# Kernel optimization log

Measured on AMD Instinct MI355X. Metric: run time of the kernel, lower is better.

## Reference

```python
import jax, jax.numpy as jnp
import numpy as np

B, L, D = 2, 2048, 1024
D_INNER, DT_RANK, D_STATE, D_CONV = 2048, 64, 16, 4


def setup_inputs() -> dict:
    key = jax.random.key(0)
    ks = jax.random.split(key, 10)
    x = jax.random.normal(ks[0], (B, L, D), jnp.float32)
    W_in = jax.random.normal(ks[1], (2 * D_INNER, D), jnp.float32) * (1.0 / np.sqrt(D))
    conv_w = jax.random.normal(ks[2], (D_INNER, 1, D_CONV), jnp.float32) * 0.5
    conv_b = jax.random.normal(ks[3], (D_INNER,), jnp.float32) * 0.1
    W_x = jax.random.normal(ks[4], (DT_RANK + 2 * D_STATE, D_INNER), jnp.float32) * (1.0 / np.sqrt(D_INNER))
    W_dt = jax.random.normal(ks[5], (D_INNER, DT_RANK), jnp.float32) * (1.0 / np.sqrt(DT_RANK))
    b_dt = jax.random.normal(ks[6], (D_INNER,), jnp.float32) * 0.1
    W_out = jax.random.normal(ks[7], (D, D_INNER), jnp.float32) * (1.0 / np.sqrt(D_INNER))
    # S4D-real style init: A_log = log(1..N) per channel
    A_log = jnp.log(jnp.tile(jnp.arange(1, D_STATE + 1, dtype=jnp.float32), (D_INNER, 1)))
    D_skip = jnp.ones((D_INNER,), jnp.float32)
    return {"x": x, "W_in": W_in, "conv_w": conv_w, "conv_b": conv_b,
            "W_x": W_x, "W_dt": W_dt, "b_dt": b_dt, "W_out": W_out,
            "A_log": A_log, "D_skip": D_skip}


def _selective_scan(xi, dt, A, Bm, Cm, D_skip):
    # xi, dt: (B,L,Di); A: (Di,N); Bm,Cm: (B,L,N); D_skip: (Di,)
    dA = jnp.exp(dt[..., None] * A)                       # (B,L,Di,N)
    dBx = dt[..., None] * Bm[:, :, None, :] * xi[..., None]  # (B,L,Di,N)

    def combine(e1, e2):
        a1, b1 = e1
        a2, b2 = e2
        return a1 * a2, a2 * b1 + b2

    _, h = jax.lax.associative_scan(combine, (dA, dBx), axis=1)  # (B,L,Di,N)
    y = jnp.einsum('bldn,bln->bld', h, Cm)
    return y + D_skip * xi


def reference(x, W_in, conv_w, conv_b, W_x, W_dt, b_dt, W_out, A_log, D_skip):
    Lq = x.shape[1]
    xz = x @ W_in.T                                   # (B,L,2*Di)
    xi, z = jnp.split(xz, 2, axis=-1)
    # causal depthwise conv over time
    xc = jnp.transpose(xi, (0, 2, 1))                 # (B,Di,L)
    xc = jax.lax.conv_general_dilated(
        xc, conv_w, window_strides=(1,), padding=[(D_CONV - 1, 0)],
        dimension_numbers=('NCH', 'OIH', 'NCH'), feature_group_count=D_INNER)
    xc = xc + conv_b[None, :, None]
    xi = jnp.transpose(xc, (0, 2, 1))[:, :Lq]         # (B,L,Di)
    xi = jax.nn.silu(xi)
    x_dbl = xi @ W_x.T                                # (B,L,dt_rank+2N)
    dt, B_ssm, C_ssm = jnp.split(x_dbl, [DT_RANK, DT_RANK + D_STATE], axis=-1)
    dt = jax.nn.softplus(dt @ W_dt.T + b_dt)          # (B,L,Di)
    A = -jnp.exp(A_log.astype(jnp.float32))
    y = _selective_scan(xi, dt, A, B_ssm, C_ssm, D_skip.astype(jnp.float32))
    return (y * jax.nn.silu(z)) @ W_out.T
```

## Files before the change

kernel.cpp:

```cpp
#include <hip/hip_runtime.h>
#include <math.h>

typedef float          floatx4  __attribute__((ext_vector_type(4)));
typedef unsigned int   uintx4   __attribute__((ext_vector_type(4)));
typedef unsigned short ushortx4 __attribute__((ext_vector_type(4)));
typedef unsigned short u16;

constexpr int Bq  = 2;
constexpr int Lq  = 2048;
constexpr int Dq  = 1024;
constexpr int DI  = 2048;
constexpr int DTR = 64;
constexpr int NST = 16;
constexpr int MR  = Bq * Lq;

constexpr size_t NWB     = (size_t)MR * DI;
constexpr size_t W_XIPRE = 0;
constexpr size_t W_Z     = NWB;
constexpr size_t W_XDBL  = 2 * NWB;
constexpr size_t SZ_XDBL = (size_t)MR * 96;
constexpr size_t SZ_PS16 = (size_t)Bq * 16 * NST * DI;
constexpr size_t W_PB    = W_XDBL + SZ_XDBL;
constexpr size_t W_SB    = W_PB + SZ_PS16;
constexpr size_t W_R1    = W_SB + SZ_PS16;
constexpr size_t W_SM    = W_R1 + NWB;
constexpr size_t U_WDT = 524288, U_WX = 655360;
constexpr size_t SM_F32  = 425984;
constexpr size_t W_PS2   = W_SM + SM_F32;
__host__ __device__ constexpr size_t SZPS(int nc) { return (size_t)Bq * nc * NST * DI; }
__host__ __device__ constexpr size_t SZR(int nc)  { return (size_t)Bq * nc * DI; }

__device__ __forceinline__ u16 f2b(float x) {
    unsigned int u = __float_as_uint(x);
    u += 0x7fffu + ((u >> 16) & 1u);
    return (u16)(u >> 16);
}
__device__ __forceinline__ float b2f(u16 h) { return __uint_as_float(((unsigned int)h) << 16); }
__device__ __forceinline__ float silu_f(float x) { return x / (1.f + __expf(-x)); }

__device__ __forceinline__ void mfma16(floatx4& d, uintx4 a, uintx4 b) {
    asm("v_mfma_f32_16x16x32_bf16 %0, %1, %2, %0" : "+v"(d) : "v"(a), "v"(b));
}
__device__ __forceinline__ void gload16(const void* g, void* l) {
    __builtin_amdgcn_global_load_lds((const __attribute__((address_space(1))) void*)g,
                                     (__attribute__((address_space(3))) void*)l, 16, 0, 0);
}

__device__ __forceinline__ void pow_ladder(float r, float dA[NST]) {
    float r2 = r * r;
    float e4 = r2 * r2;
    dA[0] = r; dA[1] = r2; dA[2] = r2 * r; dA[3] = e4;
#pragma unroll
    for (int n = 4; n < NST; n++) dA[n] = dA[n - 4] * e4;
}
__device__ __forceinline__ void dA_ladder(float dtv, float dA[NST]) {
    pow_ladder(__expf(-dtv), dA);
}
__device__ __forceinline__ float pow_m(float R, int m) {
    float r2 = R * R, r4 = r2 * r2, r8 = r4 * r4, r16 = r8 * r8;
    float p = 1.f;
    if (m & 1)  p *= R;
    if (m & 2)  p *= r2;
    if (m & 4)  p *= r4;
    if (m & 8)  p *= r8;
    if (m & 16) p *= r16;
    return p;
}

__device__ __forceinline__ void split_store(const floatx4 v, u16* hi, u16* lo, size_t t) {
    ushortx4 h, l;
#pragma unroll
    for (int i = 0; i < 4; i++) {
        h[i] = f2b(v[i]);
        l[i] = f2b(v[i] - b2f(h[i]));
    }
    ((ushortx4*)hi)[t] = h;
    ((ushortx4*)lo)[t] = l;
}
__device__ __forceinline__ void round_store(const floatx4 v, u16* hi, size_t t) {
    ushortx4 h;
#pragma unroll
    for (int i = 0; i < 4; i++) h[i] = f2b(v[i]);
    ((ushortx4*)hi)[t] = h;
}

__global__ __launch_bounds__(256)
void prep(const float* __restrict__ x, u16* __restrict__ xhi,
          const float* __restrict__ W_in, u16* __restrict__ winh,
          const float* __restrict__ W_x, u16* __restrict__ wxh,
          const float* __restrict__ W_dt, u16* __restrict__ wdth,
          float* __restrict__ xdbl,
          const float* __restrict__ W_out, u16* __restrict__ wouth)
{
    int t = blockIdx.x * 256 + threadIdx.x;
    if (t < 1048576) { round_store(((const floatx4*)x)[t], xhi, t); return; }
    t -= 1048576;
    if (t < 1048576) { round_store(((const floatx4*)W_in)[t], winh, t); return; }
    t -= 1048576;
    if (t < 49152)   { round_store(((const floatx4*)W_x)[t], wxh, t); return; }
    t -= 49152;
    if (t < 32768)   { round_store(((const floatx4*)W_dt)[t], wdth, t); return; }
    t -= 32768;
    if (t < 98304)   { ((floatx4*)xdbl)[t] = (floatx4){0.f, 0.f, 0.f, 0.f}; return; }
    t -= 98304;
    if (wouth && t < 524288) round_store(((const floatx4*)W_out)[t], wouth, t);
}

__global__ __launch_bounds__(256)
void round_bf16(const float* __restrict__ src, u16* __restrict__ hi, int n4)
{
    int t = blockIdx.x * 256 + threadIdx.x;
    if (t < n4) round_store(((const floatx4*)src)[t], hi, t);
}

__device__ __forceinline__ void stage64(const u16* g, u16* s, int rows, int ld,
                                        int k0, int wave, int lane)
{
    const int chunks = rows * 8;
    for (int c0 = wave * 64; c0 < chunks; c0 += 256) {
        int c   = c0 + lane;
        int row = c >> 3;
        int kcg = (c & 7) ^ (row & 7);
        const u16* gp = g + (size_t)row * ld + k0 + kcg * 8;
        gload16(gp, s + (size_t)c0 * 8);
    }
}

__device__ __forceinline__ void stageA_f32(const float* g, u16* sh, u16* sl,
                                           int rows, int ldf, int k0, int tid)
{
    const int chunks = rows * 8;
    for (int c = tid; c < chunks; c += 256) {
        int row = c >> 3, kc = c & 7;
        const float* gp = g + (size_t)row * ldf + k0 + kc * 8;
        floatx4 v0 = *(const floatx4*)gp;
        floatx4 v1 = *(const floatx4*)(gp + 4);
        float v[8] = {v0[0], v0[1], v0[2], v0[3], v1[0], v1[1], v1[2], v1[3]};
        unsigned int hh[8], ll[8];
#pragma unroll
        for (int i = 0; i < 8; i++) {
            u16 h = f2b(v[i]);
            hh[i] = h;
            ll[i] = f2b(v[i] - b2f(h));
        }
        uintx4 ph, pl;
#pragma unroll
        for (int i = 0; i < 4; i++) {
            ph[i] = hh[2 * i] | (hh[2 * i + 1] << 16);
            pl[i] = ll[2 * i] | (ll[2 * i + 1] << 16);
        }
        int sc = kc ^ (row & 7);
        *(uintx4*)(sh + (size_t)row * 64 + sc * 8) = ph;
        *(uintx4*)(sl + (size_t)row * 64 + sc * 8) = pl;
    }
}

template <int WM, int WN, int FM, int FN, int EPI, int AF32, int TERMS>
__global__ __launch_bounds__(256)
void gemm2t(const u16* __restrict__ Ah, const u16* __restrict__ Al,
            const u16* __restrict__ Bh,
            float* __restrict__ C, u16* __restrict__ C2u,
            const float* __restrict__ bias,
            const float* __restrict__ Af,
            int M, int N, int K, int lda, int ldb, int ldc, int nsplit)
{
    constexpr int BM = WM * FM * 16, BN = WN * FN * 16, BK = 64;
    __shared__ u16 sm[(TERMS * BM + BN) * BK];
    u16* sAh = sm;
    u16* sAl = sm + BM * BK;
    u16* sBh = sm + TERMS * BM * BK;

    const int tid = threadIdx.x, lane = tid & 63, wave = tid >> 6;
    const int wm = wave % WM, wn = wave / WM;
    const long m0 = (long)blockIdx.y * BM, n0 = (long)blockIdx.x * BN;
    const int frr = lane & 15;

    const int kchunk = K / gridDim.z;
    const int kBeg = blockIdx.z * kchunk;
    const int kEnd = kBeg + kchunk;

    floatx4 acc[FM][FN];
#pragma unroll
    for (int i = 0; i < FM; i++)
#pragma unroll
        for (int j = 0; j < FN; j++) acc[i][j] = (floatx4){0.f, 0.f, 0.f, 0.f};

    const u16* gAh = Ah + (AF32 ? 0 : (size_t)m0 * lda);
    const u16* gAl = Al + (AF32 ? 0 : (size_t)m0 * lda);
    const float* gAf = AF32 ? (Af + (size_t)m0 * lda) : nullptr;
    const u16* gBh = Bh + (size_t)n0 * ldb;

    for (int k0 = kBeg; k0 < kEnd; k0 += BK) {
        if constexpr (AF32) {
            stageA_f32(gAf, sAh, sAl, BM, lda, k0, tid);
        } else {
            stage64(gAh, sAh, BM, lda, k0, wave, lane);
            if constexpr (TERMS == 2)
                stage64(gAl, sAl, BM, lda, k0, wave, lane);
        }
        stage64(gBh, sBh, BN, ldb, k0, wave, lane);
        __syncthreads();

#pragma unroll
        for (int kk = 0; kk < 2; kk++) {
            const int kc = kk * 4 + (lane >> 4);
            uintx4 af[FM], bb[FN];
#pragma unroll
            for (int f = 0; f < FN; f++) {
                int r = (wn * FN + f) * 16 + frr;
                bb[f] = *(const uintx4*)(sBh + r * 64 + (kc ^ (r & 7)) * 8);
            }
#pragma unroll
            for (int f = 0; f < FM; f++) {
                int r = (wm * FM + f) * 16 + frr;
                af[f] = *(const uintx4*)(sAh + r * 64 + (kc ^ (r & 7)) * 8);
            }
#pragma unroll
            for (int fm = 0; fm < FM; fm++)
#pragma unroll
                for (int fn = 0; fn < FN; fn++)
                    mfma16(acc[fm][fn], af[fm], bb[fn]);
            if constexpr (TERMS == 2) {
#pragma unroll
                for (int f = 0; f < FM; f++) {
                    int r = (wm * FM + f) * 16 + frr;
                    af[f] = *(const uintx4*)(sAl + r * 64 + (kc ^ (r & 7)) * 8);
                }
#pragma unroll
                for (int fm = 0; fm < FM; fm++)
#pragma unroll
                    for (int fn = 0; fn < FN; fn++)
                        mfma16(acc[fm][fn], af[fm], bb[fn]);
            }
        }
        __syncthreads();
    }

#pragma unroll
    for (int fm = 0; fm < FM; fm++) {
        long row0 = m0 + (wm * FM + fm) * 16 + ((lane >> 4) << 2);
#pragma unroll
        for (int fn = 0; fn < FN; fn++) {
            long col = n0 + (wn * FN + fn) * 16 + (lane & 15);
#pragma unroll
            for (int i = 0; i < 4; i++) {
                long row = row0 + i;
                float v = acc[fm][fn][i];
                if constexpr (EPI == 1) {
                    v += bias[col];
                    v = (v > 20.f) ? v : log1pf(__expf(v));
                    C[row * (long)ldc + col] = v;
                } else if constexpr (EPI == 2) {
                    if (col < nsplit) C[row * (long)nsplit + col] = v;
                    else              C2u[row * (long)nsplit + (col - nsplit)] = f2b(v);
                } else if constexpr (EPI == 3) {
                    atomicAdd(&C[row * (long)ldc + col], v);
                } else {
                    C[row * (long)ldc + col] = v;
                }
            }
        }
    }
}

__global__ __launch_bounds__(256)
void conv_silu_split(const float* __restrict__ xi_pre, const float* __restrict__ cw,
                     const float* __restrict__ cb, u16* __restrict__ xih,
                     u16* __restrict__ xil)
{
    int t = blockIdx.x * 256 + threadIdx.x;
    int d4 = (t & 511) * 4;
    int l  = (t >> 9) & (Lq - 1);
    int b  = t >> 20;
    const float* base = xi_pre + ((size_t)b * Lq) * DI + d4;
    floatx4 w0 = *(const floatx4*)(cw + (size_t)(d4 + 0) * 4);
    floatx4 w1 = *(const floatx4*)(cw + (size_t)(d4 + 1) * 4);
    floatx4 w2 = *(const floatx4*)(cw + (size_t)(d4 + 2) * 4);
    floatx4 w3 = *(const floatx4*)(cw + (size_t)(d4 + 3) * 4);
    floatx4 o  = *(const floatx4*)(cb + d4);
#pragma unroll
    for (int j = 0; j < 4; j++) {
        int ls = l - 3 + j;
        if (ls < 0) continue;
        floatx4 xv = *(const floatx4*)(base + (size_t)ls * DI);
        o[0] = fmaf(w0[j], xv[0], o[0]);
        o[1] = fmaf(w1[j], xv[1], o[1]);
        o[2] = fmaf(w2[j], xv[2], o[2]);
        o[3] = fmaf(w3[j], xv[3], o[3]);
    }
    size_t oidx = ((size_t)b * Lq + l) * DI + d4;
    ushortx4 h, lo;
#pragma unroll
    for (int i = 0; i < 4; i++) {
        float v = silu_f(o[i]);
        h[i]  = f2b(v);
        lo[i] = f2b(v - b2f(h[i]));
    }
    *(ushortx4*)(xih + oidx) = h;
    *(ushortx4*)(xil + oidx) = lo;
}

template <int NCT>
__global__ __launch_bounds__(256)
void scanAY(const u16* __restrict__ xih, u16* xil ,
            const float* __restrict__ dt,
            const float* __restrict__ xdbl, const float* __restrict__ Dsk,
            u16* __restrict__ Rl16, float* __restrict__ Rend,
            float* __restrict__ S)
{
    constexpr int CLT = Lq / NCT;
    constexpr int CSH = (NCT == 64) ? 6 : (NCT == 32) ? 5 : 4;
    const int tid = threadIdx.x;
    int t = blockIdx.x * 256 + tid;
    int d = t & (DI - 1);
    int c = (t >> 11) & (NCT - 1);
    int b = t >> (11 + CSH);

    __shared__ float sBC[CLT][32];
    int l0 = c * CLT;
    {
        size_t rb = ((size_t)b * Lq + l0) * 96 + DTR;
        for (int i = tid; i < CLT * 32; i += 256) {
            int l = i >> 5, e = i & 31;
            sBC[l][e] = xdbl[rb + (size_t)l * 96 + e];
        }
    }
    __syncthreads();

    float Dv = Dsk[d];
    float h[NST];
#pragma unroll
    for (int n = 0; n < NST; n++) h[n] = 0.f;
    float R = 1.f;

    size_t xbase = ((size_t)b * Lq + l0) * DI + d;
    for (int l = 0; l < CLT; l++) {
        size_t idx = xbase + (size_t)l * DI;
        float dtv = dt[idx];
        float xiv = b2f(xih[idx]) + b2f(xil[idx]);
        float dx  = dtv * xiv;
        float dA[NST];
        dA_ladder(dtv, dA);
        R *= dA[0];
        float y = 0.f;
#pragma unroll
        for (int n = 0; n < NST; n++) {
            h[n] = fmaf(dA[n], h[n], dx * sBC[l][n]);
            y = fmaf(h[n], sBC[l][16 + n], y);
        }
        y = fmaf(Dv, xiv, y);
        xil[idx]  = f2b(y);
        Rl16[idx] = f2b(R);
    }
    Rend[((size_t)(b * NCT + c)) * DI + d] = R;
    size_t obase = ((size_t)(b * NCT + c) * NST) * DI + d;
#pragma unroll
    for (int n = 0; n < NST; n++)
        S[obase + (size_t)n * DI] = h[n];
}

template <int NCT>
__global__ __launch_bounds__(256)
void scanBt(const float* __restrict__ Rend, const float* S, float* Hin)
{
    int t = blockIdx.x * 256 + threadIdx.x;
    int d = t & (DI - 1);
    int n = (t >> 11) & (NST - 1);
    int b = t >> 15;
    const int m = n + 1;
    float H = 0.f;
    for (int c = 0; c < NCT; c++) {
        float R = Rend[((size_t)(b * NCT + c)) * DI + d];
        float p = pow_m(R, m);
        size_t idx = (((size_t)(b * NCT + c) * NST) + n) * DI + d;
        float s = S[idx];
        Hin[idx] = H;
        H = fmaf(p, H, s);
    }
}

template <int NCT>
__global__ __launch_bounds__(256)
void scanCY(u16* __restrict__ xgh,
            const u16* __restrict__ yloc16, const u16* __restrict__ Rl16,
            const float* __restrict__ xdbl,
            const float* __restrict__ Hin, const u16* __restrict__ z)
{
    constexpr int CLT = Lq / NCT;
    constexpr int CSH = (NCT == 64) ? 6 : (NCT == 32) ? 5 : 4;
    const int tid = threadIdx.x;
    int t = blockIdx.x * 256 + tid;
    int d = t & (DI - 1);
    int c = (t >> 11) & (NCT - 1);
    int b = t >> (11 + CSH);

    __shared__ float sC[CLT][NST];
    int l0 = c * CLT;
    {
        size_t rb = ((size_t)b * Lq + l0) * 96 + DTR + NST;
        for (int i = tid; i < CLT * NST; i += 256) {
            int l = i >> 4, e = i & 15;
            sC[l][e] = xdbl[rb + (size_t)l * 96 + e];
        }
    }
    __syncthreads();

    float w[NST];
    size_t hbase = ((size_t)(b * NCT + c) * NST) * DI + d;
#pragma unroll
    for (int n = 0; n < NST; n++) w[n] = Hin[hbase + (size_t)n * DI];

    size_t xbase = ((size_t)b * Lq + l0) * DI + d;
    for (int l = 0; l < CLT; l++) {
        size_t idx = xbase + (size_t)l * DI;
        float yv = b2f(yloc16[idx]);
        float Rv = b2f(Rl16[idx]);
        float pw[NST];
        pow_ladder(Rv, pw);
        float corr = 0.f;
#pragma unroll
        for (int n = 0; n < NST; n++)
            corr = fmaf(w[n] * pw[n], sC[l][n], corr);
        float y = yv + corr;
        float g = y * silu_f(b2f(z[idx]));
        xgh[idx] = f2b(g);
    }
}

extern "C" void kernel_launch(void* const* d_in, const int* in_sizes, int n_in,
                              void* d_out, int out_size, void* d_ws, size_t ws_size,
                              hipStream_t stream)
{
    const float* x      = (const float*)d_in[0];
    const float* W_in   = (const float*)d_in[1];
    const float* conv_w = (const float*)d_in[2];
    const float* conv_b = (const float*)d_in[3];
    const float* W_x    = (const float*)d_in[4];
    const float* W_dt   = (const float*)d_in[5];
    const float* b_dt   = (const float*)d_in[6];
    const float* W_out  = (const float*)d_in[7];
    const float* D_skip = (const float*)d_in[9];
    float* out = (float*)d_out;

    float* ws     = (float*)d_ws;
    float* xi_pre = ws + W_XIPRE;
    float* dt     = xi_pre;
    u16*   zb     = (u16*)(ws + W_Z);
    u16*   Rl16   = zb + NWB;
    float* xdbl   = ws + W_XDBL;
    u16* r1   = (u16*)(ws + W_R1);
    u16* xhi  = r1, *winh = r1 + 4194304;
    u16* xih  = r1, *xil = r1 + 8388608;
    u16* smal = (u16*)(ws + W_SM);
    u16* wdth = smal + U_WDT, *wxh = smal + U_WX;
    u16* wouth = (u16*)(ws + W_PB);

    int nc = 16;
    float *Rend, *Sb;
    if (ws_size >= (W_PS2 + SZR(64) + SZPS(64)) * 4) {
        nc = 64;  Rend = ws + W_PS2; Sb = Rend + SZR(64);
    } else if (ws_size >= (W_PS2 + SZR(32) + SZPS(32)) * 4) {
        nc = 32;  Rend = ws + W_PS2; Sb = Rend + SZR(32);
    } else {
        Rend = ws + W_PB; Sb = ws + W_SB;
    }
    const bool early_wout = (nc >= 32);

    prep<<<early_wout ? 10944 : 8896, 256, 0, stream>>>(
        x, xhi, W_in, winh, W_x, wxh, W_dt, wdth, xdbl,
        W_out, early_wout ? wouth : nullptr);
    gemm2t<2, 2, 4, 4, 2, 0, 1><<<dim3(32, 32), 256, 0, stream>>>(
        xhi, nullptr, winh, xi_pre, zb, nullptr, nullptr, MR, 4096, Dq, Dq, Dq, 2048, 2048);
    conv_silu_split<<<8192, 256, 0, stream>>>(xi_pre, conv_w, conv_b, xih, xil);
    gemm2t<2, 2, 4, 3, 3, 0, 2><<<dim3(1, 32, 8), 256, 0, stream>>>(
        xih, xil, wxh, xdbl, nullptr, nullptr, nullptr, MR, 96, DI, DI, DI, 96, 0);
    gemm2t<2, 2, 4, 4, 1, 1, 2><<<dim3(16, 32), 256, 0, stream>>>(
        nullptr, nullptr, wdth, dt, nullptr, b_dt, xdbl, MR, DI, DTR, 96, DTR, DI, 0);
    if (nc == 64) {
        scanAY<64><<<dim3(Bq * 64 * DI / 256), 256, 0, stream>>>(
            xih, xil, dt, xdbl, D_skip, Rl16, Rend, Sb);
        scanBt<64><<<dim3(Bq * NST * DI / 256), 256, 0, stream>>>(Rend, Sb, Sb);
        scanCY<64><<<dim3(Bq * 64 * DI / 256), 256, 0, stream>>>(
            xih, xil, Rl16, xdbl, Sb, zb);
    } else if (nc == 32) {
        scanAY<32><<<dim3(Bq * 32 * DI / 256), 256, 0, stream>>>(
            xih, xil, dt, xdbl, D_skip, Rl16, Rend, Sb);
        scanBt<32><<<dim3(Bq * NST * DI / 256), 256, 0, stream>>>(Rend, Sb, Sb);
        scanCY<32><<<dim3(Bq * 32 * DI / 256), 256, 0, stream>>>(
            xih, xil, Rl16, xdbl, Sb, zb);
    } else {
        scanAY<16><<<dim3(Bq * 16 * DI / 256), 256, 0, stream>>>(
            xih, xil, dt, xdbl, D_skip, Rl16, Rend, Sb);
        scanBt<16><<<dim3(Bq * NST * DI / 256), 256, 0, stream>>>(Rend, Sb, Sb);
        round_bf16<<<2048, 256, 0, stream>>>(W_out, wouth, 524288);
        scanCY<16><<<dim3(Bq * 16 * DI / 256), 256, 0, stream>>>(
            xih, xil, Rl16, xdbl, Sb, zb);
    }
    gemm2t<2, 2, 4, 2, 0, 0, 1><<<dim3(16, 32), 256, 0, stream>>>(
        xih, nullptr, wouth, out, nullptr, nullptr, nullptr, MR, Dq, DI, DI, DI, Dq, 0);
}
```

Measured before the change: 239.4 us.

## Store pre-conv xi as bf16 and slide conv window across time chunks

The input projection GEMM now writes the xi half in bf16 (new epilogue 4) rather than fp32, which halves that intermediate's write and read traffic. The depthwise conv kernel reads bf16 rows and each thread walks 16 consecutive time steps with a sliding three-row window. This removes the redundant re-reads of overlapping rows and uses far fewer blocks. In exchange, the pre-conv activation is rounded to bf16, which loses precision compared with the earlier fp32 path, and the conv kernel has less parallelism.

```diff
diff --git a/kernel.cpp b/kernel.cpp
--- a/kernel.cpp
+++ b/kernel.cpp
@@ -67,16 +67,6 @@
     return p;
 }
 
-__device__ __forceinline__ void split_store(const floatx4 v, u16* hi, u16* lo, size_t t) {
-    ushortx4 h, l;
-#pragma unroll
-    for (int i = 0; i < 4; i++) {
-        h[i] = f2b(v[i]);
-        l[i] = f2b(v[i] - b2f(h[i]));
-    }
-    ((ushortx4*)hi)[t] = h;
-    ((ushortx4*)lo)[t] = l;
-}
 __device__ __forceinline__ void round_store(const floatx4 v, u16* hi, size_t t) {
     ushortx4 h;
 #pragma unroll
@@ -255,6 +245,10 @@
                     else              C2u[row * (long)nsplit + (col - nsplit)] = f2b(v);
                 } else if constexpr (EPI == 3) {
                     atomicAdd(&C[row * (long)ldc + col], v);
+                } else if constexpr (EPI == 4) {
+                    u16* C1u = (u16*)C;
+                    if (col < nsplit) C1u[row * (long)nsplit + col] = f2b(v);
+                    else              C2u[row * (long)nsplit + (col - nsplit)] = f2b(v);
                 } else {
                     C[row * (long)ldc + col] = v;
                 }
@@ -264,40 +258,60 @@
 }
 
 __global__ __launch_bounds__(256)
-void conv_silu_split(const float* __restrict__ xi_pre, const float* __restrict__ cw,
+void conv_silu_split(const u16* __restrict__ xi16, const float* __restrict__ cw,
                      const float* __restrict__ cb, u16* __restrict__ xih,
                      u16* __restrict__ xil)
 {
-    int t = blockIdx.x * 256 + threadIdx.x;
-    int d4 = (t & 511) * 4;
-    int l  = (t >> 9) & (Lq - 1);
-    int b  = t >> 20;
-    const float* base = xi_pre + ((size_t)b * Lq) * DI + d4;
+    constexpr int LC = 16;
+    int t   = blockIdx.x * 256 + threadIdx.x;
+    int d4i = t & 511;
+    int lc  = (t >> 9) & 127;
+    int b   = t >> 16;
+    int d4  = d4i * 4;
+    const u16* base = xi16 + ((size_t)b * Lq) * DI + d4;
+
     floatx4 w0 = *(const floatx4*)(cw + (size_t)(d4 + 0) * 4);
     floatx4 w1 = *(const floatx4*)(cw + (size_t)(d4 + 1) * 4);
     floatx4 w2 = *(const floatx4*)(cw + (size_t)(d4 + 2) * 4);
     floatx4 w3 = *(const floatx4*)(cw + (size_t)(d4 + 3) * 4);
-    floatx4 o  = *(const floatx4*)(cb + d4);
-#pragma unroll
-    for (int j = 0; j < 4; j++) {
-        int ls = l - 3 + j;
-        if (ls < 0) continue;
-        floatx4 xv = *(const floatx4*)(base + (size_t)ls * DI);
-        o[0] = fmaf(w0[j], xv[0], o[0]);
-        o[1] = fmaf(w1[j], xv[1], o[1]);
-        o[2] = fmaf(w2[j], xv[2], o[2]);
-        o[3] = fmaf(w3[j], xv[3], o[3]);
-    }
-    size_t oidx = ((size_t)b * Lq + l) * DI + d4;
-    ushortx4 h, lo;
-#pragma unroll
-    for (int i = 0; i < 4; i++) {
-        float v = silu_f(o[i]);
-        h[i]  = f2b(v);
-        lo[i] = f2b(v - b2f(h[i]));
-    }
-    *(ushortx4*)(xih + oidx) = h;
-    *(ushortx4*)(xil + oidx) = lo;
+    floatx4 bias = *(const floatx4*)(cb + d4);
+
+    auto ldrow = [&](int l) -> floatx4 {
+        ushortx4 u = *(const ushortx4*)(base + (size_t)l * DI);
+        floatx4 r;
+#pragma unroll
+        for (int i = 0; i < 4; i++) r[i] = b2f(u[i]);
+        return r;
+    };
+    floatx4 zero = (floatx4){0.f, 0.f, 0.f, 0.f};
+    int l0 = lc * LC;
+    floatx4 xm3 = (l0 >= 3) ? ldrow(l0 - 3) : zero;
+    floatx4 xm2 = (l0 >= 2) ? ldrow(l0 - 2) : zero;
+    floatx4 xm1 = (l0 >= 1) ? ldrow(l0 - 1) : zero;
+
+    size_t obase = ((size_t)b * Lq + l0) * DI + d4;
+    for (int l = 0; l < LC; l++) {
+        floatx4 x0 = ldrow(l0 + l);
+        ushortx4 h, lo;
+#pragma unroll
+        for (int i = 0; i < 4; i++) {
+            float wv = (i == 0) ? 0.f : 0.f;
+            (void)wv;
+        }
+        float v0 = fmaf(w0[0], xm3[0], fmaf(w0[1], xm2[0], fmaf(w0[2], xm1[0], fmaf(w0[3], x0[0], bias[0]))));
+        float v1 = fmaf(w1[0], xm3[1], fmaf(w1[1], xm2[1], fmaf(w1[2], xm1[1], fmaf(w1[3], x0[1], bias[1]))));
+        float v2 = fmaf(w2[0], xm3[2], fmaf(w2[1], xm2[2], fmaf(w2[2], xm1[2], fmaf(w2[3], x0[2], bias[2]))));
+        float v3 = fmaf(w3[0], xm3[3], fmaf(w3[1], xm2[3], fmaf(w3[2], xm1[3], fmaf(w3[3], x0[3], bias[3]))));
+        float s0 = silu_f(v0), s1 = silu_f(v1), s2 = silu_f(v2), s3 = silu_f(v3);
+        h[0] = f2b(s0); lo[0] = f2b(s0 - b2f(h[0]));
+        h[1] = f2b(s1); lo[1] = f2b(s1 - b2f(h[1]));
+        h[2] = f2b(s2); lo[2] = f2b(s2 - b2f(h[2]));
+        h[3] = f2b(s3); lo[3] = f2b(s3 - b2f(h[3]));
+        size_t oidx = obase + (size_t)l * DI;
+        *(ushortx4*)(xih + oidx) = h;
+        *(ushortx4*)(xil + oidx) = lo;
+        xm3 = xm2; xm2 = xm1; xm1 = x0;
+    }
 }
 
 template <int NCT>
@@ -443,8 +457,8 @@
     float* out = (float*)d_out;
 
     float* ws     = (float*)d_ws;
-    float* xi_pre = ws + W_XIPRE;
-    float* dt     = xi_pre;
+    u16*   xi16   = (u16*)(ws + W_XIPRE);
+    float* dt     = ws + W_XIPRE;
     u16*   zb     = (u16*)(ws + W_Z);
     u16*   Rl16   = zb + NWB;
     float* xdbl   = ws + W_XDBL;
@@ -469,9 +483,9 @@
     prep<<<early_wout ? 10944 : 8896, 256, 0, stream>>>(
         x, xhi, W_in, winh, W_x, wxh, W_dt, wdth, xdbl,
         W_out, early_wout ? wouth : nullptr);
-    gemm2t<2, 2, 4, 4, 2, 0, 1><<<dim3(32, 32), 256, 0, stream>>>(
-        xhi, nullptr, winh, xi_pre, zb, nullptr, nullptr, MR, 4096, Dq, Dq, Dq, 2048, 2048);
-    conv_silu_split<<<8192, 256, 0, stream>>>(xi_pre, conv_w, conv_b, xih, xil);
+    gemm2t<2, 2, 4, 4, 4, 0, 1><<<dim3(32, 32), 256, 0, stream>>>(
+        xhi, nullptr, winh, (float*)xi16, zb, nullptr, nullptr, MR, 4096, Dq, Dq, Dq, 2048, 2048);
+    conv_silu_split<<<512, 256, 0, stream>>>(xi16, conv_w, conv_b, xih, xil);
     gemm2t<2, 2, 4, 3, 3, 0, 2><<<dim3(1, 32, 8), 256, 0, stream>>>(
         xih, xil, wxh, xdbl, nullptr, nullptr, nullptr, MR, 96, DI, DI, DI, 96, 0);
     gemm2t<2, 2, 4, 4, 1, 1, 2><<<dim3(16, 32), 256, 0, stream>>>(
```

Result: faster. 227.3 us (-5.1%).
